# Kernel tuning notes

Hardware: AMD Instinct MI355X
Metric: run time of the kernel (lower is better)

The kernel has to match this reference:

```python
import jax, jax.numpy as jnp
import numpy as np

QMAX = 127.0


def setup_inputs() -> dict:
    key = jax.random.key(0)
    k1, k2, k3, k4, k5, k6 = jax.random.split(key, 6)
    B, IN, OUT = 8192, 4096, 4096
    # Quantized activation (uint8-range values stored as float, per-sample asymmetric quant)
    x_q = jax.random.randint(k1, (B, IN), 0, 256).astype(jnp.float32)
    x_scale = jax.random.uniform(k2, (B,), dtype=jnp.float32, minval=0.001, maxval=0.02)
    x_zp = jax.random.randint(k3, (B,), 0, 256).astype(jnp.float32)
    # Symmetric per-tensor int8 weight (values in [-127, 127]) + scalar scale
    w_q = jax.random.randint(k4, (OUT, IN), -127, 128).astype(jnp.float32)
    w_scale = jax.random.uniform(k5, (1,), dtype=jnp.float32, minval=0.001, maxval=0.02)
    fp_bias = jax.random.normal(k6, (OUT,), dtype=jnp.float32)
    return {"x_q": x_q, "x_scale": x_scale, "x_zp": x_zp, "w_q": w_q,
            "w_scale": w_scale, "fp_bias": fp_bias}


def reference(x_q, x_scale, x_zp, w_q, w_scale, fp_bias):
    # zero-point subtraction (per-sample)
    xt = x_q - x_zp[:, None]                      # [B, IN]
    # integer GEMM (values are integers held in float32)
    lin = xt @ w_q.T                              # [B, OUT]
    # integer bias: round(fp_bias / (w_scale * x_scale))
    qbias = jnp.round(fp_bias[None, :] / (w_scale[0] * x_scale[:, None]))  # [B, OUT]
    lin = lin + qbias
    # requantize: symmetric per-tensor int8
    s = jnp.max(jnp.abs(lin)) / QMAX
    q = jnp.clip(jnp.round(lin / s), -QMAX, QMAX)  # [B, OUT]
    out_scale = s * x_scale * w_scale[0]           # [B]
    zero_point = jnp.zeros_like(out_scale)
    return q, out_scale, zero_point
```

## Files before the change

### kernel.cpp

```cpp
#include <hip/hip_runtime.h>
#include <hip/hip_bf16.h>


typedef int i32x4 __attribute__((ext_vector_type(4)));

#define AS1 __attribute__((address_space(1)))
#define AS3 __attribute__((address_space(3)))

__device__ __forceinline__ void async16(const void* g, void* lds) {
    __builtin_amdgcn_global_load_lds((const AS1 void*)g, (AS3 void*)lds, 16, 0, 0);
}

__global__ void conv_x_kernel(const float4* __restrict__ xq, int* __restrict__ x8,
                              int* gmax, int n4) {
    int i = blockIdx.x * 256 + threadIdx.x;
    if (i == 0) *gmax = 0;
    if (i >= n4) return;
    float4 v = xq[i];
    int b0 = ((int)v.x - 128) & 255;
    int b1 = ((int)v.y - 128) & 255;
    int b2 = ((int)v.z - 128) & 255;
    int b3 = ((int)v.w - 128) & 255;
    x8[i] = b0 | (b1 << 8) | (b2 << 16) | (b3 << 24);
}

__global__ void conv_w_kernel(const float* __restrict__ wq, int* __restrict__ w8,
                              int* __restrict__ rowsum, int K) {
    int row = blockIdx.x;
    int t = threadIdx.x;
    const float4* src = (const float4*)(wq + (size_t)row * K);
    int* dst = w8 + (size_t)row * (K >> 2);
    int sum = 0;
    int passes = K >> 10;
    for (int p = 0; p < passes; ++p) {
        float4 v = src[p * 256 + t];
        int b0 = (int)v.x, b1 = (int)v.y, b2 = (int)v.z, b3 = (int)v.w;
        sum += b0 + b1 + b2 + b3;
        dst[p * 256 + t] = (b0 & 255) | ((b1 & 255) << 8) | ((b2 & 255) << 16) | ((b3 & 255) << 24);
    }
    #pragma unroll
    for (int m = 32; m; m >>= 1) sum += __shfl_xor(sum, m, 64);
    __shared__ int wsum[4];
    if ((t & 63) == 0) wsum[t >> 6] = sum;
    __syncthreads();
    if (t == 0) rowsum[row] = wsum[0] + wsum[1] + wsum[2] + wsum[3];
}

__global__ __launch_bounds__(512, 2) void gemm_i8_kernel(
    const char* __restrict__ x8, const char* __restrict__ w8,
    const int* __restrict__ w_rowsum,
    const float* __restrict__ x_scale, const float* __restrict__ x_zp,
    const float* __restrict__ fp_bias, const float* __restrict__ w_scale_p,
    int* __restrict__ lin_out, int* gmax, int N, int K) {
    __shared__ __align__(16) char lds[4][32768];
    __shared__ int s_bmax;

    const int t = threadIdx.x;
    const int w = t >> 6, l = t & 63;
    if (t == 0) s_bmax = 0;

    const int nwg = gridDim.x;
    const int bid = blockIdx.x;
    int swz = bid;
    if ((nwg & 7) == 0) { const int cpx = nwg >> 3; swz = (bid & 7) * cpx + (bid >> 3); }
    const int ntn = N >> 8;
    const int tm = swz / ntn, tn = swz % ntn;

    const int nt = K >> 6;

    const int srow = t >> 2;
    const int phys = (t & 3) ^ ((srow >> 1) & 3);
    const char* pA0 = x8 + (size_t)(tm * 256 + srow) * K + phys * 16;
    const char* pA1 = pA0 + (size_t)128 * K;
    const char* pB0 = w8 + (size_t)(tn * 256 + srow) * K + phys * 16;
    const char* pB1 = pB0 + (size_t)128 * K;
    const int dst_t = t * 16;

    const int lane_lo = l & 15, lane_hi = l >> 4;
    const int wm = w >> 2, wn = w & 3;
    const int sl = (lane_hi ^ ((lane_lo >> 1) & 3)) << 4;
    const int abase = (wm * 128 + lane_lo) * 64 + sl;
    const int bbase = 16384 + (wn * 64 + lane_lo) * 64 + sl;

    i32x4 acc[8][4] = {};

    #pragma unroll
    for (int g = 0; g < 3; ++g) {
        char* buf = lds[g];
        const size_t koff = (size_t)g * 64;
        async16(pA0 + koff, buf + dst_t);
        async16(pA1 + koff, buf + 8192 + dst_t);
        async16(pB0 + koff, buf + 16384 + dst_t);
        async16(pB1 + koff, buf + 24576 + dst_t);
    }

    for (int j = 0; j < nt; ++j) {
        if (j + 2 < nt)       asm volatile("s_waitcnt vmcnt(8)" ::: "memory");
        else if (j + 2 == nt) asm volatile("s_waitcnt vmcnt(4)" ::: "memory");
        else                  asm volatile("s_waitcnt vmcnt(0)" ::: "memory");
        __builtin_amdgcn_s_barrier();
        if (j + 3 < nt) {
            char* buf = lds[(j + 3) & 3];
            const size_t koff = (size_t)(j + 3) * 64;
            async16(pA0 + koff, buf + dst_t);
            async16(pA1 + koff, buf + 8192 + dst_t);
            async16(pB0 + koff, buf + 16384 + dst_t);
            async16(pB1 + koff, buf + 24576 + dst_t);
        }
        const char* buf = lds[j & 3];
        i32x4 bf[4], af[8];
        #pragma unroll
        for (int n = 0; n < 4; ++n) bf[n] = *(const i32x4*)(buf + bbase + n * 1024);
        #pragma unroll
        for (int m = 0; m < 8; ++m) af[m] = *(const i32x4*)(buf + abase + m * 1024);
        __builtin_amdgcn_s_setprio(1);
        #pragma unroll
        for (int m = 0; m < 8; ++m)
            #pragma unroll
            for (int n = 0; n < 4; ++n)
                acc[m][n] = __builtin_amdgcn_mfma_i32_16x16x64_i8(af[m], bf[n], acc[m][n], 0, 0, 0);
        __builtin_amdgcn_s_setprio(0);
    }

    const float ws = *w_scale_p;
    const int rowg0 = tm * 256 + wm * 128 + lane_hi * 4;
    const int colg0 = tn * 256 + wn * 64 + lane_lo;
    float fb[4]; int wrs[4];
    #pragma unroll
    for (int n = 0; n < 4; ++n) {
        fb[n] = fp_bias[colg0 + n * 16];
        wrs[n] = w_rowsum[colg0 + n * 16];
    }
    int lmax = 0;
    #pragma unroll
    for (int m = 0; m < 8; ++m) {
        #pragma unroll
        for (int r = 0; r < 4; ++r) {
            const int row = rowg0 + m * 16 + r;
            const float xs = x_scale[row];
            const int zz = 128 - (int)x_zp[row];
            const float d = ws * xs;
            int* orow = lin_out + (size_t)row * N + colg0;
            #pragma unroll
            for (int n = 0; n < 4; ++n) {
                const int qb = (int)rintf(fb[n] / d);
                const int lin = acc[m][n][r] + zz * wrs[n] + qb;
                const int a = lin < 0 ? -lin : lin;
                lmax = a > lmax ? a : lmax;
                orow[n * 16] = lin;
            }
        }
    }
    atomicMax(&s_bmax, lmax);
    __syncthreads();
    if (t == 0) atomicMax(gmax, s_bmax);
}

__global__ void requant_kernel(float4* qout, const int4* lin, const int* gmax, int n4) {
    int i = blockIdx.x * 256 + threadIdx.x;
    if (i >= n4) return;
    float s = (float)(*gmax) / 127.0f;
    int4 v = lin[i];
    float4 o;
    o.x = fminf(127.0f, fmaxf(-127.0f, rintf((float)v.x / s)));
    o.y = fminf(127.0f, fmaxf(-127.0f, rintf((float)v.y / s)));
    o.z = fminf(127.0f, fmaxf(-127.0f, rintf((float)v.z / s)));
    o.w = fminf(127.0f, fmaxf(-127.0f, rintf((float)v.w / s)));
    qout[i] = o;
}

__global__ void scale_kernel(float* __restrict__ out_scale, float* __restrict__ out_zp,
                             const float* __restrict__ x_scale,
                             const float* __restrict__ w_scale_p,
                             const int* gmax, int B) {
    int i = blockIdx.x * 256 + threadIdx.x;
    if (i >= B) return;
    float s = (float)(*gmax) / 127.0f;
    out_scale[i] = s * x_scale[i] * w_scale_p[0];
    out_zp[i] = 0.0f;
}

extern "C" void kernel_launch(void* const* d_in, const int* in_sizes, int n_in,
                              void* d_out, int out_size, void* d_ws, size_t ws_size,
                              hipStream_t stream) {
    const float* x_q     = (const float*)d_in[0];
    const float* x_scale = (const float*)d_in[1];
    const float* x_zp    = (const float*)d_in[2];
    const float* w_q     = (const float*)d_in[3];
    const float* w_scale = (const float*)d_in[4];
    const float* fp_bias = (const float*)d_in[5];

    const int B   = in_sizes[1];
    const int IN  = in_sizes[0] / B;
    const int OUT = in_sizes[5];

    float* q         = (float*)d_out;
    float* out_scale = q + (size_t)B * OUT;
    float* out_zp    = out_scale + B;

    char* ws    = (char*)d_ws;
    int* gmax   = (int*)ws;
    char* x8    = ws + 64;
    char* w8    = x8 + (size_t)B * IN;
    int* rowsum = (int*)(w8 + (size_t)OUT * IN);
    size_t needed = 64 + (size_t)B * IN + (size_t)OUT * IN + (size_t)OUT * 4;
    if (ws_size < needed) return;

    int n4x = (B * IN) >> 2;
    conv_x_kernel<<<(n4x + 255) / 256, 256, 0, stream>>>((const float4*)x_q, (int*)x8, gmax, n4x);
    conv_w_kernel<<<OUT, 256, 0, stream>>>(w_q, (int*)w8, rowsum, IN);

    int nblocks = (B / 256) * (OUT / 256);
    gemm_i8_kernel<<<nblocks, 512, 0, stream>>>(x8, w8, rowsum, x_scale, x_zp, fp_bias,
                                                w_scale, (int*)q, gmax, OUT, IN);

    int n4q = (B * OUT) >> 2;
    requant_kernel<<<(n4q + 255) / 256, 256, 0, stream>>>((float4*)q, (const int4*)q, gmax, n4q);
    scale_kernel<<<(B + 255) / 256, 256, 0, stream>>>(out_scale, out_zp, x_scale, w_scale, gmax, B);
}
```

Before: 273.6 us.

## Interleave LDS reads, async loads and MFMA in four barrier-synced phases

Restructures the int8 GEMM main loop into four phases per K-step. Each phase issues a subset of LDS fragment reads and one async global-to-LDS load, then runs a quarter of the MFMAs, with barriers and priority raised around the math to keep the waves in lockstep (ping-pong style). The LDS ring drops from 4 to 3 buffers with prefetch depth 2, and launch bounds drop to 1 block per CU, which gives each wave more registers. The intent is to overlap memory traffic with matrix math more finely and to cut register pressure from holding all fragments at once. The cost is many more barriers per iteration and lower occupancy.

```diff
diff --git a/kernel.cpp b/kernel.cpp
--- a/kernel.cpp
+++ b/kernel.cpp
@@ -46,13 +46,23 @@
     if (t == 0) rowsum[row] = wsum[0] + wsum[1] + wsum[2] + wsum[3];
 }
 
-__global__ __launch_bounds__(512, 2) void gemm_i8_kernel(
+#define PHASE_SYNC()                                        \
+    __builtin_amdgcn_s_barrier();                           \
+    asm volatile("s_waitcnt lgkmcnt(0)" ::: "memory");      \
+    __builtin_amdgcn_sched_barrier(0);                      \
+    __builtin_amdgcn_s_setprio(1)
+
+#define PHASE_END()                                         \
+    __builtin_amdgcn_s_setprio(0);                          \
+    __builtin_amdgcn_s_barrier()
+
+__global__ __launch_bounds__(512, 1) void gemm_i8_kernel(
     const char* __restrict__ x8, const char* __restrict__ w8,
     const int* __restrict__ w_rowsum,
     const float* __restrict__ x_scale, const float* __restrict__ x_zp,
     const float* __restrict__ fp_bias, const float* __restrict__ w_scale_p,
     int* __restrict__ lin_out, int* gmax, int N, int K) {
-    __shared__ __align__(16) char lds[4][32768];
+    __shared__ __align__(16) char lds[3][32768];
     __shared__ int s_bmax;
 
     const int t = threadIdx.x;
@@ -83,9 +93,10 @@
     const int bbase = 16384 + (wn * 64 + lane_lo) * 64 + sl;
 
     i32x4 acc[8][4] = {};
-
-    #pragma unroll
-    for (int g = 0; g < 3; ++g) {
+    i32x4 af[4], bf[4];
+
+    #pragma unroll
+    for (int g = 0; g < 2; ++g) {
         char* buf = lds[g];
         const size_t koff = (size_t)g * 64;
         async16(pA0 + koff, buf + dst_t);
@@ -93,33 +104,66 @@
         async16(pB0 + koff, buf + 16384 + dst_t);
         async16(pB1 + koff, buf + 24576 + dst_t);
     }
-
+    asm volatile("s_waitcnt vmcnt(4)" ::: "memory");
+    __builtin_amdgcn_s_barrier();
+
+    int cur = 0, stg = 2;
     for (int j = 0; j < nt; ++j) {
-        if (j + 2 < nt)       asm volatile("s_waitcnt vmcnt(8)" ::: "memory");
-        else if (j + 2 == nt) asm volatile("s_waitcnt vmcnt(4)" ::: "memory");
-        else                  asm volatile("s_waitcnt vmcnt(0)" ::: "memory");
+        const char* buf = lds[cur];
+        char* sbuf = lds[stg];
+        const size_t koff2 = (size_t)(j + 2) << 6;
+        const bool more = (j + 2) < nt;
+
+        #pragma unroll
+        for (int m = 0; m < 4; ++m) af[m] = *(const i32x4*)(buf + abase + m * 1024);
+        bf[0] = *(const i32x4*)(buf + bbase);
+        bf[1] = *(const i32x4*)(buf + bbase + 1024);
+        if (more) async16(pA0 + koff2, sbuf + dst_t);
+        PHASE_SYNC();
+        #pragma unroll
+        for (int m = 0; m < 4; ++m) {
+            acc[m][0] = __builtin_amdgcn_mfma_i32_16x16x64_i8(af[m], bf[0], acc[m][0], 0, 0, 0);
+            acc[m][1] = __builtin_amdgcn_mfma_i32_16x16x64_i8(af[m], bf[1], acc[m][1], 0, 0, 0);
+        }
+        PHASE_END();
+
+        bf[2] = *(const i32x4*)(buf + bbase + 2048);
+        bf[3] = *(const i32x4*)(buf + bbase + 3072);
+        if (more) async16(pA1 + koff2, sbuf + 8192 + dst_t);
+        PHASE_SYNC();
+        #pragma unroll
+        for (int m = 0; m < 4; ++m) {
+            acc[m][2] = __builtin_amdgcn_mfma_i32_16x16x64_i8(af[m], bf[2], acc[m][2], 0, 0, 0);
+            acc[m][3] = __builtin_amdgcn_mfma_i32_16x16x64_i8(af[m], bf[3], acc[m][3], 0, 0, 0);
+        }
+        PHASE_END();
+
+        #pragma unroll
+        for (int m = 0; m < 4; ++m) af[m] = *(const i32x4*)(buf + abase + (m + 4) * 1024);
+        if (more) async16(pB0 + koff2, sbuf + 16384 + dst_t);
+        PHASE_SYNC();
+        #pragma unroll
+        for (int m = 0; m < 4; ++m) {
+            acc[m + 4][0] = __builtin_amdgcn_mfma_i32_16x16x64_i8(af[m], bf[0], acc[m + 4][0], 0, 0, 0);
+            acc[m + 4][1] = __builtin_amdgcn_mfma_i32_16x16x64_i8(af[m], bf[1], acc[m + 4][1], 0, 0, 0);
+        }
+        PHASE_END();
+
+        if (more) async16(pB1 + koff2, sbuf + 24576 + dst_t);
         __builtin_amdgcn_s_barrier();
-        if (j + 3 < nt) {
-            char* buf = lds[(j + 3) & 3];
-            const size_t koff = (size_t)(j + 3) * 64;
-            async16(pA0 + koff, buf + dst_t);
-            async16(pA1 + koff, buf + 8192 + dst_t);
-            async16(pB0 + koff, buf + 16384 + dst_t);
-            async16(pB1 + koff, buf + 24576 + dst_t);
-        }
-        const char* buf = lds[j & 3];
-        i32x4 bf[4], af[8];
-        #pragma unroll
-        for (int n = 0; n < 4; ++n) bf[n] = *(const i32x4*)(buf + bbase + n * 1024);
-        #pragma unroll
-        for (int m = 0; m < 8; ++m) af[m] = *(const i32x4*)(buf + abase + m * 1024);
         __builtin_amdgcn_s_setprio(1);
         #pragma unroll
-        for (int m = 0; m < 8; ++m)
-            #pragma unroll
-            for (int n = 0; n < 4; ++n)
-                acc[m][n] = __builtin_amdgcn_mfma_i32_16x16x64_i8(af[m], bf[n], acc[m][n], 0, 0, 0);
+        for (int m = 0; m < 4; ++m) {
+            acc[m + 4][2] = __builtin_amdgcn_mfma_i32_16x16x64_i8(af[m], bf[2], acc[m + 4][2], 0, 0, 0);
+            acc[m + 4][3] = __builtin_amdgcn_mfma_i32_16x16x64_i8(af[m], bf[3], acc[m + 4][3], 0, 0, 0);
+        }
         __builtin_amdgcn_s_setprio(0);
+        if (j + 2 < nt)       asm volatile("s_waitcnt vmcnt(4)" ::: "memory");
+        else if (j + 1 < nt)  asm volatile("s_waitcnt vmcnt(0)" ::: "memory");
+        __builtin_amdgcn_s_barrier();
+
+        cur = (cur == 2) ? 0 : cur + 1;
+        stg = (stg == 2) ? 0 : stg + 1;
     }
 
     const float ws = *w_scale_p;
```

Measured after the change: 270.6 us. About the same (-1.1%).

## Shrink int8 GEMM tile to 128x128 with 256 threads and triple buffering

Applied to the files above, without the earlier changes.

Reworks the int8 MFMA GEMM from 256x256 tiles with 512 threads and a 4-deep LDS ring to 128x128 tiles with 256 threads, a 3-deep ring and one fewer stage of prefetch lookahead. This quadruples the block count and lowers LDS use per block, aiming for more concurrent blocks per CU and better load balance. The cost is lower arithmetic intensity and more global traffic per MFMA. The epilogue also replaces a per-element division for the quantized bias with a multiply by a precomputed reciprocal. That can change rounding of round(fp_bias/(ws*xs)) near half-integers.

```diff
diff --git a/kernel.cpp b/kernel.cpp
--- a/kernel.cpp
+++ b/kernel.cpp
@@ -46,13 +46,13 @@
     if (t == 0) rowsum[row] = wsum[0] + wsum[1] + wsum[2] + wsum[3];
 }
 
-__global__ __launch_bounds__(512, 2) void gemm_i8_kernel(
+__global__ __launch_bounds__(256, 3) void gemm_i8_kernel(
     const char* __restrict__ x8, const char* __restrict__ w8,
     const int* __restrict__ w_rowsum,
     const float* __restrict__ x_scale, const float* __restrict__ x_zp,
     const float* __restrict__ fp_bias, const float* __restrict__ w_scale_p,
     int* __restrict__ lin_out, int* gmax, int N, int K) {
-    __shared__ __align__(16) char lds[4][32768];
+    __shared__ __align__(16) char lds[3][16384];
     __shared__ int s_bmax;
 
     const int t = threadIdx.x;
@@ -60,90 +60,91 @@
     if (t == 0) s_bmax = 0;
 
     const int nwg = gridDim.x;
-    const int bid = blockIdx.x;
-    int swz = bid;
-    if ((nwg & 7) == 0) { const int cpx = nwg >> 3; swz = (bid & 7) * cpx + (bid >> 3); }
-    const int ntn = N >> 8;
+    int swz = blockIdx.x;
+    if ((nwg & 7) == 0) { const int cpx = nwg >> 3; swz = (swz & 7) * cpx + (swz >> 3); }
+    const int ntn = N >> 7;
     const int tm = swz / ntn, tn = swz % ntn;
 
     const int nt = K >> 6;
 
     const int srow = t >> 2;
     const int phys = (t & 3) ^ ((srow >> 1) & 3);
-    const char* pA0 = x8 + (size_t)(tm * 256 + srow) * K + phys * 16;
-    const char* pA1 = pA0 + (size_t)128 * K;
-    const char* pB0 = w8 + (size_t)(tn * 256 + srow) * K + phys * 16;
-    const char* pB1 = pB0 + (size_t)128 * K;
+    const char* pA0 = x8 + (size_t)(tm * 128 + srow) * K + phys * 16;
+    const char* pA1 = pA0 + (size_t)64 * K;
+    const char* pB0 = w8 + (size_t)(tn * 128 + srow) * K + phys * 16;
+    const char* pB1 = pB0 + (size_t)64 * K;
     const int dst_t = t * 16;
 
     const int lane_lo = l & 15, lane_hi = l >> 4;
-    const int wm = w >> 2, wn = w & 3;
-    const int sl = (lane_hi ^ ((lane_lo >> 1) & 3)) << 4;
-    const int abase = (wm * 128 + lane_lo) * 64 + sl;
-    const int bbase = 16384 + (wn * 64 + lane_lo) * 64 + sl;
-
-    i32x4 acc[8][4] = {};
-
-    #pragma unroll
-    for (int g = 0; g < 3; ++g) {
+    const int wm = w >> 1, wn = w & 1;
+    const int ar = wm * 64 + lane_lo;
+    const int aoff = ar * 64 + ((lane_hi ^ ((ar >> 1) & 3)) << 4);
+    const int br = wn * 64 + lane_lo;
+    const int boff = 8192 + br * 64 + ((lane_hi ^ ((br >> 1) & 3)) << 4);
+
+    i32x4 acc[4][4] = {};
+
+    #pragma unroll
+    for (int g = 0; g < 2; ++g) {
         char* buf = lds[g];
         const size_t koff = (size_t)g * 64;
         async16(pA0 + koff, buf + dst_t);
-        async16(pA1 + koff, buf + 8192 + dst_t);
-        async16(pB0 + koff, buf + 16384 + dst_t);
-        async16(pB1 + koff, buf + 24576 + dst_t);
-    }
-
+        async16(pA1 + koff, buf + 4096 + dst_t);
+        async16(pB0 + koff, buf + 8192 + dst_t);
+        async16(pB1 + koff, buf + 12288 + dst_t);
+    }
+
+    int cur = 0, stg = 2;
     for (int j = 0; j < nt; ++j) {
-        if (j + 2 < nt)       asm volatile("s_waitcnt vmcnt(8)" ::: "memory");
-        else if (j + 2 == nt) asm volatile("s_waitcnt vmcnt(4)" ::: "memory");
-        else                  asm volatile("s_waitcnt vmcnt(0)" ::: "memory");
+        if (j + 1 < nt) asm volatile("s_waitcnt vmcnt(4)" ::: "memory");
+        else            asm volatile("s_waitcnt vmcnt(0)" ::: "memory");
         __builtin_amdgcn_s_barrier();
-        if (j + 3 < nt) {
-            char* buf = lds[(j + 3) & 3];
-            const size_t koff = (size_t)(j + 3) * 64;
-            async16(pA0 + koff, buf + dst_t);
-            async16(pA1 + koff, buf + 8192 + dst_t);
-            async16(pB0 + koff, buf + 16384 + dst_t);
-            async16(pB1 + koff, buf + 24576 + dst_t);
+        if (j + 2 < nt) {
+            char* sb = lds[stg];
+            const size_t koff = (size_t)(j + 2) << 6;
+            async16(pA0 + koff, sb + dst_t);
+            async16(pA1 + koff, sb + 4096 + dst_t);
+            async16(pB0 + koff, sb + 8192 + dst_t);
+            async16(pB1 + koff, sb + 12288 + dst_t);
         }
-        const char* buf = lds[j & 3];
-        i32x4 bf[4], af[8];
-        #pragma unroll
-        for (int n = 0; n < 4; ++n) bf[n] = *(const i32x4*)(buf + bbase + n * 1024);
-        #pragma unroll
-        for (int m = 0; m < 8; ++m) af[m] = *(const i32x4*)(buf + abase + m * 1024);
+        const char* buf = lds[cur];
+        i32x4 af[4], bf[4];
+        #pragma unroll
+        for (int n = 0; n < 4; ++n) bf[n] = *(const i32x4*)(buf + boff + n * 1024);
+        #pragma unroll
+        for (int m = 0; m < 4; ++m) af[m] = *(const i32x4*)(buf + aoff + m * 1024);
         __builtin_amdgcn_s_setprio(1);
         #pragma unroll
-        for (int m = 0; m < 8; ++m)
+        for (int m = 0; m < 4; ++m)
             #pragma unroll
             for (int n = 0; n < 4; ++n)
                 acc[m][n] = __builtin_amdgcn_mfma_i32_16x16x64_i8(af[m], bf[n], acc[m][n], 0, 0, 0);
         __builtin_amdgcn_s_setprio(0);
+        cur = (cur == 2) ? 0 : cur + 1;
+        stg = (stg == 2) ? 0 : stg + 1;
     }
 
     const float ws = *w_scale_p;
-    const int rowg0 = tm * 256 + wm * 128 + lane_hi * 4;
-    const int colg0 = tn * 256 + wn * 64 + lane_lo;
-    float fb[4]; int wrs[4];
+    const int rowg0 = tm * 128 + wm * 64 + lane_hi * 4;
+    const int colg0 = tn * 128 + wn * 64 + lane_lo;
+    float fbws[4]; int wrs[4];
     #pragma unroll
     for (int n = 0; n < 4; ++n) {
-        fb[n] = fp_bias[colg0 + n * 16];
+        fbws[n] = fp_bias[colg0 + n * 16] / ws;
         wrs[n] = w_rowsum[colg0 + n * 16];
     }
     int lmax = 0;
     #pragma unroll
-    for (int m = 0; m < 8; ++m) {
+    for (int m = 0; m < 4; ++m) {
         #pragma unroll
         for (int r = 0; r < 4; ++r) {
             const int row = rowg0 + m * 16 + r;
-            const float xs = x_scale[row];
+            const float rxs = 1.0f / x_scale[row];
             const int zz = 128 - (int)x_zp[row];
-            const float d = ws * xs;
             int* orow = lin_out + (size_t)row * N + colg0;
             #pragma unroll
             for (int n = 0; n < 4; ++n) {
-                const int qb = (int)rintf(fb[n] / d);
+                const int qb = (int)rintf(fbws[n] * rxs);
                 const int lin = acc[m][n][r] + zz * wrs[n] + qb;
                 const int a = lin < 0 ? -lin : lin;
                 lmax = a > lmax ? a : lmax;
@@ -210,8 +211,8 @@
     conv_x_kernel<<<(n4x + 255) / 256, 256, 0, stream>>>((const float4*)x_q, (int*)x8, gmax, n4x);
     conv_w_kernel<<<OUT, 256, 0, stream>>>(w_q, (int*)w8, rowsum, IN);
 
-    int nblocks = (B / 256) * (OUT / 256);
-    gemm_i8_kernel<<<nblocks, 512, 0, stream>>>(x8, w8, rowsum, x_scale, x_zp, fp_bias,
+    int nblocks = (B / 128) * (OUT / 128);
+    gemm_i8_kernel<<<nblocks, 256, 0, stream>>>(x8, w8, rowsum, x_scale, x_zp, fp_bias,
                                                 w_scale, (int*)q, gmax, OUT, IN);
 
     int n4q = (B * OUT) >> 2;
```

Result: no change. 277.6 us (+1.4%).
